# Kernel optimization log

Measured on AMD Instinct MI355X. Metric: run time of the kernel, lower is better.

Reference implementation:

```python
import jax, jax.numpy as jnp
import numpy as np

N_SRC = 100000
N_DST = 50000
N_EDGES = 600000
D = 128


def setup_inputs() -> dict:
    key = jax.random.key(0)
    k1, k2, k3, k4, k5 = jax.random.split(key, 5)
    src_rep = jax.random.normal(k1, (N_SRC, D), dtype=jnp.float32)
    dst_rep = jax.random.normal(k2, (N_DST, D), dtype=jnp.float32)
    edge_src = jax.random.randint(k3, (N_EDGES,), 0, N_SRC, dtype=jnp.int64)
    edge_dst = jax.random.randint(k4, (N_EDGES,), 0, N_DST, dtype=jnp.int64)
    W = jax.random.normal(k5, (2 * D, D), dtype=jnp.float32) * (1.0 / np.sqrt(2 * D))
    b = jnp.zeros((D,), dtype=jnp.float32)
    return {"src_rep": src_rep, "dst_rep": dst_rep, "edge_src": edge_src,
            "edge_dst": edge_dst, "W": W, "b": b}


def reference(src_rep, dst_rep, edge_src, edge_dst, W, b):
    # copy_src: gather source reps along edges  [E, D]
    msgs = src_rep[edge_src]
    # sum reduce: scatter-add messages to destination nodes  [N_dst, D]
    agg = jax.ops.segment_sum(msgs, edge_dst, num_segments=dst_rep.shape[0])
    # NodeUpdater: concat(dst rep, summed messages) -> Linear -> activation
    # (Dropout is identity in eval mode.)
    concat = jnp.concatenate([dst_rep, agg], axis=1)  # [N_dst, 2D]
    new_rep = jax.nn.relu(concat @ W + b)  # [N_dst, D]
    return new_rep
```

## Files before the change

kernel.cpp:

```cpp
#include <hip/hip_runtime.h>

#define N_SRC   100000
#define N_DST   50000
#define N_EDGES 600000
#define D       128
#define RPB     16
#define PAD     48

typedef short bf16x8 __attribute__((ext_vector_type(8)));
typedef float f32x4  __attribute__((ext_vector_type(4)));

static __device__ __forceinline__ unsigned short f2bf(float f) {
    unsigned u = __float_as_uint(f);
    u += 0x7FFF + ((u >> 16) & 1);
    return (unsigned short)(u >> 16);
}
static __device__ __forceinline__ unsigned pk(float a, float b) {
    return (unsigned)f2bf(a) | ((unsigned)f2bf(b) << 16);
}

__global__ __launch_bounds__(256) void prep_kernel(
    const float* __restrict__ W, unsigned short* __restrict__ Wt,
    int* __restrict__ cnt) {
    int t = blockIdx.x * 256 + threadIdx.x;
    if (t < 2 * D * D) {
        int n = t >> 8, k = t & 255;
        Wt[n * 256 + k] = f2bf(W[(size_t)k * D + n]);
    }
    int c = t - 2 * D * D;
    if (c >= 0 && c < N_DST) cnt[c] = 0;
}

__global__ __launch_bounds__(256) void fill_kernel(
    const int* __restrict__ edge_src, const int* __restrict__ edge_dst,
    int* __restrict__ cnt, int* __restrict__ perm) {
    int e = blockIdx.x * 256 + threadIdx.x;
    if (e < N_EDGES) {
        int d = edge_dst[e];
        int pos = atomicAdd(&cnt[d], 1);
        if (pos < PAD) perm[d * PAD + pos] = edge_src[e];
    }
}

__global__ __launch_bounds__(256) void gather_kernel(
    const float* __restrict__ src_rep,
    const int*   __restrict__ cnt,
    const int*   __restrict__ perm,
    unsigned short* __restrict__ agg) {
    const int tid = threadIdx.x, lane = tid & 63, wave = tid >> 6;
    const int h = lane >> 5, c = lane & 31;
    const int dn = blockIdx.x * 4 + wave;
    const int deg = min(cnt[dn], PAD);
    const int pi = perm[(size_t)dn * PAD + min(lane, PAD - 1)];

    f32x4 a0 = {0.f, 0.f, 0.f, 0.f}, a1 = a0, a2 = a0, a3 = a0;
    const int dm1 = deg - 1;
    for (int base = 0; base < deg; base += 8) {
        int e0 = base + h, e1 = base + 2 + h, e2 = base + 4 + h, e3 = base + 6 + h;
        int s0 = __shfl(pi, min(e0, dm1));
        int s1 = __shfl(pi, min(e1, dm1));
        int s2 = __shfl(pi, min(e2, dm1));
        int s3 = __shfl(pi, min(e3, dm1));
        if (e0 <= dm1) a0 += *reinterpret_cast<const f32x4*>(src_rep + (size_t)s0 * D + c * 4);
        if (e1 <= dm1) a1 += *reinterpret_cast<const f32x4*>(src_rep + (size_t)s1 * D + c * 4);
        if (e2 <= dm1) a2 += *reinterpret_cast<const f32x4*>(src_rep + (size_t)s2 * D + c * 4);
        if (e3 <= dm1) a3 += *reinterpret_cast<const f32x4*>(src_rep + (size_t)s3 * D + c * 4);
    }
    a0 += a1; a2 += a3; a0 += a2;
#pragma unroll
    for (int q = 0; q < 4; ++q) a0[q] += __shfl_xor(a0[q], 32);
    if (h == 0) {
        uint2 w;
        w.x = pk(a0[0], a0[1]); w.y = pk(a0[2], a0[3]);
        *reinterpret_cast<uint2*>(agg + (size_t)dn * D + c * 4) = w;
    }
}

__global__ __launch_bounds__(256) void gemm_kernel(
    const float* __restrict__ dst_rep,
    const unsigned short* __restrict__ agg,
    const unsigned short* __restrict__ Wt,
    const float* __restrict__ bias,
    float*       __restrict__ out) {
    __shared__ unsigned short Abf[RPB * 2 * D];
    const int row0 = blockIdx.x * RPB;
    const int tid = threadIdx.x, lane = tid & 63, wave = tid >> 6;

    {
        int r = tid >> 4, b = tid & 15;
        const float4* p = reinterpret_cast<const float4*>(
            dst_rep + (size_t)(row0 + r) * D + b * 8);
        float4 v0 = p[0], v1 = p[1];
        uint4 w;
        w.x = pk(v0.x, v0.y); w.y = pk(v0.z, v0.w);
        w.z = pk(v1.x, v1.y); w.w = pk(v1.z, v1.w);
        *reinterpret_cast<uint4*>(&Abf[r * 256 + (b ^ (r & 7)) * 8]) = w;
        uint4 g = *reinterpret_cast<const uint4*>(agg + (size_t)(row0 + r) * D + b * 8);
        *reinterpret_cast<uint4*>(&Abf[r * 256 + ((16 + b) ^ (r & 7)) * 8]) = g;
    }
    __syncthreads();

    f32x4 c0 = {0.f, 0.f, 0.f, 0.f}, c1 = {0.f, 0.f, 0.f, 0.f};
    const int ar = lane & 15;
    const int kb = lane >> 4;
    const int n0 = wave * 32 + (lane & 15);
#pragma unroll
    for (int s = 0; s < 8; ++s) {
        int b = s * 4 + kb;
        bf16x8 af = *reinterpret_cast<const bf16x8*>(&Abf[ar * 256 + (b ^ (ar & 7)) * 8]);
        int kbase = s * 32 + kb * 8;
        bf16x8 b0 = *reinterpret_cast<const bf16x8*>(&Wt[(size_t)n0 * 256 + kbase]);
        bf16x8 b1 = *reinterpret_cast<const bf16x8*>(&Wt[(size_t)(n0 + 16) * 256 + kbase]);
        c0 = __builtin_amdgcn_mfma_f32_16x16x32_bf16(af, b0, c0, 0, 0, 0);
        c1 = __builtin_amdgcn_mfma_f32_16x16x32_bf16(af, b1, c1, 0, 0, 0);
    }

    const float bv0 = bias[wave * 32 + (lane & 15)];
    const float bv1 = bias[wave * 32 + 16 + (lane & 15)];
#pragma unroll
    for (int g = 0; g < 4; ++g) {
        size_t orow = row0 + (lane >> 4) * 4 + g;
        out[orow * D + wave * 32 + (lane & 15)]      = fmaxf(c0[g] + bv0, 0.f);
        out[orow * D + wave * 32 + 16 + (lane & 15)] = fmaxf(c1[g] + bv1, 0.f);
    }
}

extern "C" void kernel_launch(void* const* d_in, const int* in_sizes, int n_in,
                              void* d_out, int out_size, void* d_ws, size_t ws_size,
                              hipStream_t stream) {
    const float* src_rep  = (const float*)d_in[0];
    const float* dst_rep  = (const float*)d_in[1];
    const int*   edge_src = (const int*)d_in[2];
    const int*   edge_dst = (const int*)d_in[3];
    const float* W        = (const float*)d_in[4];
    const float* bias     = (const float*)d_in[5];
    float*       out      = (float*)d_out;

    int* cnt  = (int*)d_ws;
    int* perm = cnt + N_DST;
    size_t wt_off = (((size_t)N_DST * (1 + PAD) * 4 + 255) / 256) * 256;
    unsigned short* Wt  = (unsigned short*)((char*)d_ws + wt_off);
    unsigned short* agg = Wt + (size_t)2 * D * D;

    prep_kernel<<<(2 * D * D + N_DST + 255) / 256, 256, 0, stream>>>(W, Wt, cnt);
    fill_kernel<<<(N_EDGES + 255) / 256, 256, 0, stream>>>(edge_src, edge_dst, cnt, perm);
    gather_kernel<<<N_DST / 4, 256, 0, stream>>>(src_rep, cnt, perm, agg);
    gemm_kernel<<<N_DST / RPB, 256, 0, stream>>>(dst_rep, agg, Wt, bias, out);
}
```

Before: 118.0 us.

## Pre-convert source reps to bf16 and gather packed bf16 rows

Adds a pass that converts all of src_rep to bf16 in workspace, launched in the same kernel as the edge-bucketing fill. The gather then reads 16-byte bf16 chunks per lane, four edges per wave step, with cross-quarter shuffle reduction. This halves the bytes per gathered row. In exchange it adds a full read of src_rep plus a half-size write, and rounds messages to bf16 before summation. The old f32 path remains as a fallback when the workspace is too small.

```diff
diff --git a/kernel.cpp b/kernel.cpp
--- a/kernel.cpp
+++ b/kernel.cpp
@@ -7,6 +7,10 @@
 #define RPB     16
 #define PAD     48
 
+#define CONV_THREADS ((N_SRC * D) / 8)
+#define CONV_BLOCKS  (CONV_THREADS / 256)
+#define FILL_BLOCKS  ((N_EDGES + 255) / 256)
+
 typedef short bf16x8 __attribute__((ext_vector_type(8)));
 typedef float f32x4  __attribute__((ext_vector_type(4)));
 
@@ -17,6 +21,16 @@
 }
 static __device__ __forceinline__ unsigned pk(float a, float b) {
     return (unsigned)f2bf(a) | ((unsigned)f2bf(b) << 16);
+}
+static __device__ __forceinline__ void addpk(float* a, uint4 u) {
+    a[0] += __uint_as_float(u.x << 16);
+    a[1] += __uint_as_float(u.x & 0xFFFF0000u);
+    a[2] += __uint_as_float(u.y << 16);
+    a[3] += __uint_as_float(u.y & 0xFFFF0000u);
+    a[4] += __uint_as_float(u.z << 16);
+    a[5] += __uint_as_float(u.z & 0xFFFF0000u);
+    a[6] += __uint_as_float(u.w << 16);
+    a[7] += __uint_as_float(u.w & 0xFFFF0000u);
 }
 
 __global__ __launch_bounds__(256) void prep_kernel(
@@ -29,6 +43,28 @@
     }
     int c = t - 2 * D * D;
     if (c >= 0 && c < N_DST) cnt[c] = 0;
+}
+
+__global__ __launch_bounds__(256) void convfill_kernel(
+    const float* __restrict__ src_rep, unsigned short* __restrict__ srcb,
+    const int* __restrict__ edge_src, const int* __restrict__ edge_dst,
+    int* __restrict__ cnt, int* __restrict__ perm) {
+    if (blockIdx.x < CONV_BLOCKS) {
+        int t = blockIdx.x * 256 + threadIdx.x;
+        const float4* p = reinterpret_cast<const float4*>(src_rep) + (size_t)t * 2;
+        float4 v0 = p[0], v1 = p[1];
+        uint4 w;
+        w.x = pk(v0.x, v0.y); w.y = pk(v0.z, v0.w);
+        w.z = pk(v1.x, v1.y); w.w = pk(v1.z, v1.w);
+        reinterpret_cast<uint4*>(srcb)[t] = w;
+    } else {
+        int e = (blockIdx.x - CONV_BLOCKS) * 256 + threadIdx.x;
+        if (e < N_EDGES) {
+            int d = edge_dst[e];
+            int pos = atomicAdd(&cnt[d], 1);
+            if (pos < PAD) perm[d * PAD + pos] = edge_src[e];
+        }
+    }
 }
 
 __global__ __launch_bounds__(256) void fill_kernel(
@@ -42,7 +78,47 @@
     }
 }
 
-__global__ __launch_bounds__(256) void gather_kernel(
+__global__ __launch_bounds__(256) void gather_bf16_kernel(
+    const unsigned short* __restrict__ srcb,
+    const int* __restrict__ cnt,
+    const int* __restrict__ perm,
+    unsigned short* __restrict__ agg) {
+    const int tid = threadIdx.x, lane = tid & 63, wave = tid >> 6;
+    const int q = lane >> 4, cl = lane & 15;
+    const int dn = blockIdx.x * 4 + wave;
+    const int deg = min(cnt[dn], PAD);
+    const int pi = perm[(size_t)dn * PAD + min(lane, PAD - 1)];
+    const int dm1 = deg - 1;
+
+    float a0[8] = {0,0,0,0,0,0,0,0}, a1[8] = {0,0,0,0,0,0,0,0};
+    for (int base = 0; base < deg; base += 16) {
+        int e0 = base + q, e1 = base + 4 + q, e2 = base + 8 + q, e3 = base + 12 + q;
+        int s0 = __shfl(pi, min(e0, dm1));
+        int s1 = __shfl(pi, min(e1, dm1));
+        int s2 = __shfl(pi, min(e2, dm1));
+        int s3 = __shfl(pi, min(e3, dm1));
+        uint4 u0 = {0,0,0,0}, u1 = {0,0,0,0}, u2 = {0,0,0,0}, u3 = {0,0,0,0};
+        if (e0 <= dm1) u0 = *reinterpret_cast<const uint4*>(srcb + (size_t)s0 * D + cl * 8);
+        if (e1 <= dm1) u1 = *reinterpret_cast<const uint4*>(srcb + (size_t)s1 * D + cl * 8);
+        if (e2 <= dm1) u2 = *reinterpret_cast<const uint4*>(srcb + (size_t)s2 * D + cl * 8);
+        if (e3 <= dm1) u3 = *reinterpret_cast<const uint4*>(srcb + (size_t)s3 * D + cl * 8);
+        addpk(a0, u0); addpk(a1, u1); addpk(a0, u2); addpk(a1, u3);
+    }
+#pragma unroll
+    for (int i = 0; i < 8; ++i) {
+        a0[i] += a1[i];
+        a0[i] += __shfl_xor(a0[i], 16);
+        a0[i] += __shfl_xor(a0[i], 32);
+    }
+    if (lane < 16) {
+        uint4 w;
+        w.x = pk(a0[0], a0[1]); w.y = pk(a0[2], a0[3]);
+        w.z = pk(a0[4], a0[5]); w.w = pk(a0[6], a0[7]);
+        *reinterpret_cast<uint4*>(agg + (size_t)dn * D + cl * 8) = w;
+    }
+}
+
+__global__ __launch_bounds__(256) void gather_f32_kernel(
     const float* __restrict__ src_rep,
     const int*   __restrict__ cnt,
     const int*   __restrict__ perm,
@@ -68,7 +144,7 @@
     }
     a0 += a1; a2 += a3; a0 += a2;
 #pragma unroll
-    for (int q = 0; q < 4; ++q) a0[q] += __shfl_xor(a0[q], 32);
+    for (int qq = 0; qq < 4; ++qq) a0[qq] += __shfl_xor(a0[qq], 32);
     if (h == 0) {
         uint2 w;
         w.x = pk(a0[0], a0[1]); w.y = pk(a0[2], a0[3]);
@@ -139,11 +215,20 @@
     int* cnt  = (int*)d_ws;
     int* perm = cnt + N_DST;
     size_t wt_off = (((size_t)N_DST * (1 + PAD) * 4 + 255) / 256) * 256;
-    unsigned short* Wt  = (unsigned short*)((char*)d_ws + wt_off);
-    unsigned short* agg = Wt + (size_t)2 * D * D;
+    unsigned short* Wt   = (unsigned short*)((char*)d_ws + wt_off);
+    unsigned short* agg  = Wt + (size_t)2 * D * D;
+    unsigned short* srcb = agg + (size_t)N_DST * D;
+    const size_t need_full = wt_off + ((size_t)2 * D * D + (size_t)N_DST * D
+                             + (size_t)N_SRC * D) * sizeof(unsigned short);
 
     prep_kernel<<<(2 * D * D + N_DST + 255) / 256, 256, 0, stream>>>(W, Wt, cnt);
-    fill_kernel<<<(N_EDGES + 255) / 256, 256, 0, stream>>>(edge_src, edge_dst, cnt, perm);
-    gather_kernel<<<N_DST / 4, 256, 0, stream>>>(src_rep, cnt, perm, agg);
+    if (ws_size >= need_full) {
+        convfill_kernel<<<CONV_BLOCKS + FILL_BLOCKS, 256, 0, stream>>>(
+            src_rep, srcb, edge_src, edge_dst, cnt, perm);
+        gather_bf16_kernel<<<N_DST / 4, 256, 0, stream>>>(srcb, cnt, perm, agg);
+    } else {
+        fill_kernel<<<FILL_BLOCKS, 256, 0, stream>>>(edge_src, edge_dst, cnt, perm);
+        gather_f32_kernel<<<N_DST / 4, 256, 0, stream>>>(src_rep, cnt, perm, agg);
+    }
     gemm_kernel<<<N_DST / RPB, 256, 0, stream>>>(dst_rep, agg, Wt, bias, out);
 }
```

Result: no change. 118.6 us (+0.5%).

## Fuse gather and GEMM with async global-to-LDS double-buffered edge loads

Applied to the files above, without the earlier changes.

Merges the gather and GEMM kernels into one 512-thread block per 16 destination rows, so the aggregated rows go straight into shared memory instead of through a bf16 global buffer. Each wave gathers two rows using global_load_lds into a double-buffered LDS stage, with manual waitcnt pipelining. Out-of-range edges are pointed at a zeroed row. The fill kernel now handles two edges per thread with vectorised loads. The trade-off is fewer edges in flight per wave (two per round instead of eight), plus inline-asm scheduling that is fragile.

```diff
diff --git a/kernel.cpp b/kernel.cpp
--- a/kernel.cpp
+++ b/kernel.cpp
@@ -4,8 +4,11 @@
 #define N_DST   50000
 #define N_EDGES 600000
 #define D       128
-#define RPB     16
 #define PAD     48
+
+#define MISC_ELEMS   (2 * D * D + N_DST + D)
+#define MISC_BLOCKS  ((MISC_ELEMS + 255) / 256)
+#define FILL_BLOCKS  ((N_EDGES / 2 + 255) / 256)
 
 typedef short bf16x8 __attribute__((ext_vector_type(8)));
 typedef float f32x4  __attribute__((ext_vector_type(4)));
@@ -21,7 +24,7 @@
 
 __global__ __launch_bounds__(256) void prep_kernel(
     const float* __restrict__ W, unsigned short* __restrict__ Wt,
-    int* __restrict__ cnt) {
+    int* __restrict__ cnt, float* __restrict__ zrow) {
     int t = blockIdx.x * 256 + threadIdx.x;
     if (t < 2 * D * D) {
         int n = t >> 8, k = t & 255;
@@ -29,64 +32,48 @@
     }
     int c = t - 2 * D * D;
     if (c >= 0 && c < N_DST) cnt[c] = 0;
+    int z = c - N_DST;
+    if (z >= 0 && z < D) zrow[z] = 0.f;
 }
 
 __global__ __launch_bounds__(256) void fill_kernel(
     const int* __restrict__ edge_src, const int* __restrict__ edge_dst,
     int* __restrict__ cnt, int* __restrict__ perm) {
-    int e = blockIdx.x * 256 + threadIdx.x;
-    if (e < N_EDGES) {
-        int d = edge_dst[e];
-        int pos = atomicAdd(&cnt[d], 1);
-        if (pos < PAD) perm[d * PAD + pos] = edge_src[e];
+    int e0 = (blockIdx.x * 256 + threadIdx.x) * 2;
+    if (e0 < N_EDGES) {
+        int2 s2 = *reinterpret_cast<const int2*>(edge_src + e0);
+        int2 d2 = *reinterpret_cast<const int2*>(edge_dst + e0);
+        int p0 = atomicAdd(&cnt[d2.x], 1);
+        if (p0 < PAD) perm[d2.x * PAD + p0] = s2.x;
+        int p1 = atomicAdd(&cnt[d2.y], 1);
+        if (p1 < PAD) perm[d2.y * PAD + p1] = s2.y;
     }
 }
 
-__global__ __launch_bounds__(256) void gather_kernel(
+__global__ __launch_bounds__(512) void fused_kernel(
     const float* __restrict__ src_rep,
+    const float* __restrict__ dst_rep,
     const int*   __restrict__ cnt,
     const int*   __restrict__ perm,
-    unsigned short* __restrict__ agg) {
-    const int tid = threadIdx.x, lane = tid & 63, wave = tid >> 6;
-    const int h = lane >> 5, c = lane & 31;
-    const int dn = blockIdx.x * 4 + wave;
-    const int deg = min(cnt[dn], PAD);
-    const int pi = perm[(size_t)dn * PAD + min(lane, PAD - 1)];
-
-    f32x4 a0 = {0.f, 0.f, 0.f, 0.f}, a1 = a0, a2 = a0, a3 = a0;
-    const int dm1 = deg - 1;
-    for (int base = 0; base < deg; base += 8) {
-        int e0 = base + h, e1 = base + 2 + h, e2 = base + 4 + h, e3 = base + 6 + h;
-        int s0 = __shfl(pi, min(e0, dm1));
-        int s1 = __shfl(pi, min(e1, dm1));
-        int s2 = __shfl(pi, min(e2, dm1));
-        int s3 = __shfl(pi, min(e3, dm1));
-        if (e0 <= dm1) a0 += *reinterpret_cast<const f32x4*>(src_rep + (size_t)s0 * D + c * 4);
-        if (e1 <= dm1) a1 += *reinterpret_cast<const f32x4*>(src_rep + (size_t)s1 * D + c * 4);
-        if (e2 <= dm1) a2 += *reinterpret_cast<const f32x4*>(src_rep + (size_t)s2 * D + c * 4);
-        if (e3 <= dm1) a3 += *reinterpret_cast<const f32x4*>(src_rep + (size_t)s3 * D + c * 4);
-    }
-    a0 += a1; a2 += a3; a0 += a2;
-#pragma unroll
-    for (int q = 0; q < 4; ++q) a0[q] += __shfl_xor(a0[q], 32);
-    if (h == 0) {
-        uint2 w;
-        w.x = pk(a0[0], a0[1]); w.y = pk(a0[2], a0[3]);
-        *reinterpret_cast<uint2*>(agg + (size_t)dn * D + c * 4) = w;
-    }
-}
-
-__global__ __launch_bounds__(256) void gemm_kernel(
-    const float* __restrict__ dst_rep,
-    const unsigned short* __restrict__ agg,
+    const float* __restrict__ zrow,
     const unsigned short* __restrict__ Wt,
     const float* __restrict__ bias,
     float*       __restrict__ out) {
-    __shared__ unsigned short Abf[RPB * 2 * D];
-    const int row0 = blockIdx.x * RPB;
+    __shared__ __align__(16) f32x4 stage[8][2][2][64];
+    __shared__ unsigned short Abf[16 * 256];
+    const int row0 = blockIdx.x * 16;
     const int tid = threadIdx.x, lane = tid & 63, wave = tid >> 6;
+    const int h = lane >> 5, c = lane & 31;
 
-    {
+    const int dn0 = row0 + wave * 2;
+    const int2 cc = *reinterpret_cast<const int2*>(&cnt[dn0]);
+    const int dmA = min(cc.x, PAD) - 1, dmB = min(cc.y, PAD) - 1;
+    const int dcA = max(dmA, 0), dcB = max(dmB, 0);
+    const int piA = perm[(size_t)dn0 * PAD + min(lane, PAD - 1)];
+    const int piB = perm[(size_t)(dn0 + 1) * PAD + min(lane, PAD - 1)];
+    const int rounds = (max(dmA, dmB) + 2) >> 1;
+
+    if (tid < 256) {
         int r = tid >> 4, b = tid & 15;
         const float4* p = reinterpret_cast<const float4*>(
             dst_rep + (size_t)(row0 + r) * D + b * 8);
@@ -95,33 +82,75 @@
         w.x = pk(v0.x, v0.y); w.y = pk(v0.z, v0.w);
         w.z = pk(v1.x, v1.y); w.w = pk(v1.z, v1.w);
         *reinterpret_cast<uint4*>(&Abf[r * 256 + (b ^ (r & 7)) * 8]) = w;
-        uint4 g = *reinterpret_cast<const uint4*>(agg + (size_t)(row0 + r) * D + b * 8);
-        *reinterpret_cast<uint4*>(&Abf[r * 256 + ((16 + b) ^ (r & 7)) * 8]) = g;
+    }
+
+    f32x4 accA = {0.f, 0.f, 0.f, 0.f}, accB = accA;
+    auto ISSUE = [&](int rd, int slot) {
+        int e = rd * 2 + h;
+        int rA = __shfl(piA, min(e, dcA));
+        int rB = __shfl(piB, min(e, dcB));
+        const float* pA = (e <= dmA) ? (src_rep + (size_t)rA * D) : zrow;
+        const float* pB = (e <= dmB) ? (src_rep + (size_t)rB * D) : zrow;
+        __builtin_amdgcn_global_load_lds(
+            (const unsigned int*)(pA + c * 4),
+            (unsigned int*)(&stage[wave][slot][0][0]), 16, 0, 0);
+        __builtin_amdgcn_global_load_lds(
+            (const unsigned int*)(pB + c * 4),
+            (unsigned int*)(&stage[wave][slot][1][0]), 16, 0, 0);
+    };
+    auto CONSUME = [&](int slot) {
+        accA += stage[wave][slot][0][lane];
+        accB += stage[wave][slot][1][lane];
+    };
+
+    if (rounds > 0) {
+        ISSUE(0, 0);
+        for (int rd = 0; rd + 1 < rounds; ++rd) {
+            ISSUE(rd + 1, (rd + 1) & 1);
+            asm volatile("s_waitcnt vmcnt(2)" ::: "memory");
+            __builtin_amdgcn_sched_barrier(0);
+            CONSUME(rd & 1);
+            asm volatile("s_waitcnt lgkmcnt(0)" ::: "memory");
+            __builtin_amdgcn_sched_barrier(0);
+        }
+        asm volatile("s_waitcnt vmcnt(0)" ::: "memory");
+        __builtin_amdgcn_sched_barrier(0);
+        CONSUME((rounds - 1) & 1);
+    }
+
+#pragma unroll
+    for (int i = 0; i < 4; ++i) {
+        accA[i] += __shfl_xor(accA[i], 32);
+        accB[i] += __shfl_xor(accB[i], 32);
+    }
+    if (h == 0) {
+        const int rA = wave * 2, rB = wave * 2 + 1;
+        int b = 16 + (c >> 1);
+        uint2 w0, w1;
+        w0.x = pk(accA[0], accA[1]); w0.y = pk(accA[2], accA[3]);
+        w1.x = pk(accB[0], accB[1]); w1.y = pk(accB[2], accB[3]);
+        *reinterpret_cast<uint2*>(&Abf[rA * 256 + (b ^ (rA & 7)) * 8 + (c & 1) * 4]) = w0;
+        *reinterpret_cast<uint2*>(&Abf[rB * 256 + (b ^ (rB & 7)) * 8 + (c & 1) * 4]) = w1;
     }
     __syncthreads();
 
-    f32x4 c0 = {0.f, 0.f, 0.f, 0.f}, c1 = {0.f, 0.f, 0.f, 0.f};
+    f32x4 c0 = {0.f, 0.f, 0.f, 0.f};
     const int ar = lane & 15;
     const int kb = lane >> 4;
-    const int n0 = wave * 32 + (lane & 15);
+    const int n0 = wave * 16 + (lane & 15);
 #pragma unroll
     for (int s = 0; s < 8; ++s) {
         int b = s * 4 + kb;
         bf16x8 af = *reinterpret_cast<const bf16x8*>(&Abf[ar * 256 + (b ^ (ar & 7)) * 8]);
-        int kbase = s * 32 + kb * 8;
-        bf16x8 b0 = *reinterpret_cast<const bf16x8*>(&Wt[(size_t)n0 * 256 + kbase]);
-        bf16x8 b1 = *reinterpret_cast<const bf16x8*>(&Wt[(size_t)(n0 + 16) * 256 + kbase]);
+        bf16x8 b0 = *reinterpret_cast<const bf16x8*>(&Wt[(size_t)n0 * 256 + s * 32 + kb * 8]);
         c0 = __builtin_amdgcn_mfma_f32_16x16x32_bf16(af, b0, c0, 0, 0, 0);
-        c1 = __builtin_amdgcn_mfma_f32_16x16x32_bf16(af, b1, c1, 0, 0, 0);
     }
 
-    const float bv0 = bias[wave * 32 + (lane & 15)];
-    const float bv1 = bias[wave * 32 + 16 + (lane & 15)];
+    const float bv = bias[n0];
 #pragma unroll
     for (int g = 0; g < 4; ++g) {
         size_t orow = row0 + (lane >> 4) * 4 + g;
-        out[orow * D + wave * 32 + (lane & 15)]      = fmaxf(c0[g] + bv0, 0.f);
-        out[orow * D + wave * 32 + 16 + (lane & 15)] = fmaxf(c1[g] + bv1, 0.f);
+        out[orow * D + n0] = fmaxf(c0[g] + bv, 0.f);
     }
 }
 
@@ -139,11 +168,11 @@
     int* cnt  = (int*)d_ws;
     int* perm = cnt + N_DST;
     size_t wt_off = (((size_t)N_DST * (1 + PAD) * 4 + 255) / 256) * 256;
-    unsigned short* Wt  = (unsigned short*)((char*)d_ws + wt_off);
-    unsigned short* agg = Wt + (size_t)2 * D * D;
+    unsigned short* Wt = (unsigned short*)((char*)d_ws + wt_off);
+    float* zrow = (float*)(Wt + (size_t)2 * D * D);
 
-    prep_kernel<<<(2 * D * D + N_DST + 255) / 256, 256, 0, stream>>>(W, Wt, cnt);
-    fill_kernel<<<(N_EDGES + 255) / 256, 256, 0, stream>>>(edge_src, edge_dst, cnt, perm);
-    gather_kernel<<<N_DST / 4, 256, 0, stream>>>(src_rep, cnt, perm, agg);
-    gemm_kernel<<<N_DST / RPB, 256, 0, stream>>>(dst_rep, agg, Wt, bias, out);
+    prep_kernel<<<MISC_BLOCKS, 256, 0, stream>>>(W, Wt, cnt, zrow);
+    fill_kernel<<<FILL_BLOCKS, 256, 0, stream>>>(edge_src, edge_dst, cnt, perm);
+    fused_kernel<<<N_DST / 16, 512, 0, stream>>>(
+        src_rep, dst_rep, cnt, perm, zrow, Wt, bias, out);
 }
```

New measurement: 106.5 us. 1.11x faster.
